# Performance work log

Hardware: AMD Instinct MI355X
Metric: run time of the kernel (lower is better)

Reference implementation:

```python
import jax, jax.numpy as jnp
import numpy as np

# DkNetCL (ConformalLayers): depth x [Conv2d(3x3, pad=1, no bias) + SRePro], then Linear(32768 -> 10).
# ConformalLayers algebraically fuses the cascade in conformal space; the equivalent Euclidean math
# per layer is: x <- conv(x); x <- x * 2*alpha^2 / (2*alpha^2 + ||x||^2), where ||x|| is the l2 norm
# of the ENTIRE flattened feature map of each sample (the sample is a single point in conformal space).
# alpha fixed to 1.0 (cl.SRePro() default is weight-adaptive; a constant keeps the reference deterministic).

DEPTH = 4
ALPHA = 1.0


def _conv(x, w):
    # x: [B, Cin, H, W], w: [Cout, Cin, 3, 3], stride 1, padding 1 (shape-preserving)
    return jax.lax.conv_general_dilated(
        x, w, window_strides=(1, 1), padding=((1, 1), (1, 1)),
        dimension_numbers=("NCHW", "OIHW", "NCHW"))


def _srepro(x, alpha):
    # per-sample squared norm over the whole feature map
    sq = jnp.sum(x * x, axis=(1, 2, 3), keepdims=True)  # [B,1,1,1]
    two_a2 = 2.0 * alpha * alpha
    return x * (two_a2 / (two_a2 + sq))


def setup_inputs() -> dict:
    key = jax.random.key(0)
    ks = jax.random.split(key, DEPTH + 2)
    B, H, W = 1024, 32, 32
    x = jax.random.normal(ks[0], (B, 3, H, W), jnp.float32)
    inp = {"x": x}
    cin = 3
    for i in range(DEPTH):
        fan_in = cin * 9
        inp[f"conv_w{i}"] = jax.random.normal(ks[1 + i], (32, cin, 3, 3), jnp.float32) / np.sqrt(fan_in).astype(np.float32)
        cin = 32
    flat = 32 * H * W  # 32768
    inp["fc_w"] = jax.random.normal(ks[-1], (10, flat), jnp.float32) / np.sqrt(flat).astype(np.float32)
    inp["fc_b"] = jnp.zeros((10,), jnp.float32)
    return inp


def reference(x, conv_w0, conv_w1, conv_w2, conv_w3, fc_w, fc_b):
    for w in (conv_w0, conv_w1, conv_w2, conv_w3):
        x = _srepro(_conv(x, w), ALPHA)
    x = x.reshape(x.shape[0], -1)  # [B, 32768]
    return x @ fc_w.T + fc_b  # [B, 10]
```

## Files before the change

kernel.cpp:

```cpp
#include <hip/hip_runtime.h>
#include <stdint.h>


typedef __bf16 bf16x8 __attribute__((ext_vector_type(8)));
typedef float f32x4 __attribute__((ext_vector_type(4)));
typedef unsigned short u16;
typedef unsigned int u32;

__device__ __forceinline__ u16 f2bf(float f) {
    union { float f; u32 i; } v; v.f = f;
    u32 r = v.i + 0x7FFFu + ((v.i >> 16) & 1u);
    return (u16)(r >> 16);
}
__device__ __forceinline__ float bf2f(u16 u) {
    union { u32 i; float f; } v; v.i = ((u32)u) << 16;
    return v.f;
}
union frag_cast { uint4 u; bf16x8 f; };

__device__ __forceinline__ int swz(int p, int c) {
    return p * 32 + ((c ^ ((p >> 1) & 3)) * 8);
}

__global__ void prep_weights_k(const float* __restrict__ w0, const float* __restrict__ w1,
                               const float* __restrict__ w2, const float* __restrict__ w3,
                               u16* __restrict__ wfrag)
{
    int idx = blockIdx.x * 256 + threadIdx.x;
    if (idx >= 4 * 9 * 2 * 64) return;
    int lane  = idx & 63;
    int mh    = (idx >> 6) & 1;
    int tap   = (idx >> 7) % 9;
    int layer = (idx >> 7) / 9;
    const float* w = layer == 0 ? w0 : layer == 1 ? w1 : layer == 2 ? w2 : w3;
    int cin_act = (layer == 0) ? 3 : 32;
    int cout = mh * 16 + (lane & 15);
    int cin0 = (lane >> 4) * 8;
    int dy = tap / 3, dx = tap % 3;
    u16 v[8];
    for (int j = 0; j < 8; j++) {
        int cin = cin0 + j;
        float f = (cin < cin_act) ? w[((cout * cin_act + cin) * 3 + dy) * 3 + dx] : 0.f;
        v[j] = f2bf(f);
    }
    uint4 pack;
    pack.x = (u32)v[0] | ((u32)v[1] << 16);
    pack.y = (u32)v[2] | ((u32)v[3] << 16);
    pack.z = (u32)v[4] | ((u32)v[5] << 16);
    pack.w = (u32)v[6] | ((u32)v[7] << 16);
    reinterpret_cast<uint4*>(wfrag)[idx] = pack;
}

__global__ void prep_wfc_k(const float* __restrict__ fcw, u16* __restrict__ wfc)
{
    int idx = blockIdx.x * 256 + threadIdx.x;
    int lane = idx & 63, step = idx >> 6;
    int j = lane & 15, kq = lane >> 4;
    u16 hi[8], lo[8];
#pragma unroll
    for (int e = 0; e < 8; e++) {
        int k = step * 32 + kq * 8 + e;
        int c = k & 31, p = k >> 5;
        float f = (j < 10) ? fcw[j * 32768 + c * 1024 + p] : 0.f;
        u16 h = f2bf(f);
        hi[e] = h;
        lo[e] = f2bf(f - bf2f(h));
    }
    uint4 ph, pl;
    ph.x = (u32)hi[0] | ((u32)hi[1] << 16); ph.y = (u32)hi[2] | ((u32)hi[3] << 16);
    ph.z = (u32)hi[4] | ((u32)hi[5] << 16); ph.w = (u32)hi[6] | ((u32)hi[7] << 16);
    pl.x = (u32)lo[0] | ((u32)lo[1] << 16); pl.y = (u32)lo[2] | ((u32)lo[3] << 16);
    pl.z = (u32)lo[4] | ((u32)lo[5] << 16); pl.w = (u32)lo[6] | ((u32)lo[7] << 16);
    reinterpret_cast<uint4*>(wfc)[idx] = ph;
    reinterpret_cast<uint4*>(wfc)[65536 + idx] = pl;
}

__global__ void __launch_bounds__(512, 1)
net_k(const float* __restrict__ x, const u16* __restrict__ wfrag,
      u16* __restrict__ u4, float* __restrict__ c4)
{
    __shared__ u16 lds[2][32768];
    __shared__ float red[8][4];
    const int b = blockIdx.x;
    const int tid = threadIdx.x;
    const int lane = tid & 63;
    const int wv = tid >> 6;
    const int px = lane & 15;
    const int kq = lane >> 4;
    float vn[4] = {0.f, 0.f, 0.f, 0.f};

    const float* xb = x + (size_t)b * 3072;
#pragma unroll
    for (int it = 0; it < 8; it++) {
        int pix = it * 128 + wv * 16 + px;
        int c = kq;
        uint4 val = make_uint4(0, 0, 0, 0);
        if (c == 0) {
            float f0 = xb[pix], f1 = xb[1024 + pix], f2 = xb[2048 + pix];
            val.x = (u32)f2bf(f0) | ((u32)f2bf(f1) << 16);
            val.y = (u32)f2bf(f2);
        }
        *reinterpret_cast<uint4*>(&lds[0][swz(pix, c)]) = val;
    }

    const int orow0 = wv * 4;
#pragma unroll 1
    for (int l = 0; l < 4; l++) {
        bf16x8 W[3][3][2];
        const uint4* wl = reinterpret_cast<const uint4*>(wfrag + l * 9216);
#pragma unroll
        for (int dy = 0; dy < 3; dy++)
#pragma unroll
            for (int dx = 0; dx < 3; dx++)
#pragma unroll
                for (int mh = 0; mh < 2; mh++) {
                    frag_cast fc;
                    fc.u = wl[((dy * 3 + dx) * 2 + mh) * 64 + lane];
                    W[dy][dx][mh] = fc.f;
                }
        const u16* src = lds[l & 1];
        u16* dst = lds[(l & 1) ^ 1];
        __syncthreads();

#pragma unroll 1
        for (int ch = 0; ch < 2; ch++) {
            const int oA = orow0 + ch * 2;
            f32x4 accA[2][2]; f32x4 accB[2][2];
#pragma unroll
            for (int mh = 0; mh < 2; mh++)
#pragma unroll
                for (int nt = 0; nt < 2; nt++) { accA[mh][nt] = (f32x4)0.f; accB[mh][nt] = (f32x4)0.f; }

#pragma unroll
            for (int k = 0; k < 4; k++) {
                int ri = oA - 1 + k;
                if (ri >= 0 && ri < 32) {
                    bf16x8 bfr[2][3];
#pragma unroll
                    for (int nt = 0; nt < 2; nt++)
#pragma unroll
                        for (int d = 0; d < 3; d++) {
                            int xx = nt * 16 + px + d - 1;
                            bool oob = ((unsigned)xx >= 32u);
                            int xc = oob ? (nt * 16 + px) : xx;
                            frag_cast fc;
                            fc.u = *reinterpret_cast<const uint4*>(&src[swz(ri * 32 + xc, kq)]);
                            if (oob) { fc.u.x = 0; fc.u.y = 0; fc.u.z = 0; fc.u.w = 0; }
                            bfr[nt][d] = fc.f;
                        }
                    if (k <= 2) {
#pragma unroll
                        for (int mh = 0; mh < 2; mh++)
#pragma unroll
                            for (int nt = 0; nt < 2; nt++)
#pragma unroll
                                for (int d = 0; d < 3; d++)
                                    accA[mh][nt] = __builtin_amdgcn_mfma_f32_16x16x32_bf16(
                                        W[k][d][mh], bfr[nt][d], accA[mh][nt], 0, 0, 0);
                    }
                    if (k >= 1) {
#pragma unroll
                        for (int mh = 0; mh < 2; mh++)
#pragma unroll
                            for (int nt = 0; nt < 2; nt++)
#pragma unroll
                                for (int d = 0; d < 3; d++)
                                    accB[mh][nt] = __builtin_amdgcn_mfma_f32_16x16x32_bf16(
                                        W[k - 1][d][mh], bfr[nt][d], accB[mh][nt], 0, 0, 0);
                    }
                }
            }
#pragma unroll
            for (int mh = 0; mh < 2; mh++)
#pragma unroll
                for (int nt = 0; nt < 2; nt++) {
                    int cch = mh * 2 + (kq >> 1);
                    int sub = (kq & 1) * 4;
                    f32x4 a = accA[mh][nt];
                    vn[l] += a[0]*a[0] + a[1]*a[1] + a[2]*a[2] + a[3]*a[3];
                    ushort4 h = make_ushort4(f2bf(a[0]), f2bf(a[1]), f2bf(a[2]), f2bf(a[3]));
                    int P0 = oA * 32 + nt * 16 + px;
                    *reinterpret_cast<ushort4*>(&dst[swz(P0, cch) + sub]) = h;
                    f32x4 c = accB[mh][nt];
                    vn[l] += c[0]*c[0] + c[1]*c[1] + c[2]*c[2] + c[3]*c[3];
                    ushort4 h2 = make_ushort4(f2bf(c[0]), f2bf(c[1]), f2bf(c[2]), f2bf(c[3]));
                    int P1 = (oA + 1) * 32 + nt * 16 + px;
                    *reinterpret_cast<ushort4*>(&dst[swz(P1, cch) + sub]) = h2;
                }
        }
    }

#pragma unroll
    for (int l = 0; l < 4; l++)
#pragma unroll
        for (int off = 32; off; off >>= 1) vn[l] += __shfl_xor(vn[l], off);
    if (lane == 0) {
#pragma unroll
        for (int l = 0; l < 4; l++) red[wv][l] = vn[l];
    }
    __syncthreads();
    float c = 1.f;
#pragma unroll
    for (int l = 0; l < 4; l++) {
        float n = 0.f;
#pragma unroll
        for (int w = 0; w < 8; w++) n += red[w][l];
        c = c * (2.f / (2.f + c * c * n));
    }
    if (tid == 0) c4[b] = c;

    u16* ub = u4 + (size_t)b * 32768;
#pragma unroll
    for (int it = 0; it < 8; it++) {
        int pix = it * 128 + wv * 16 + px;
        int cch = kq;
        *reinterpret_cast<uint4*>(ub + pix * 32 + cch * 8) =
            *reinterpret_cast<const uint4*>(&lds[0][swz(pix, cch)]);
    }
}

__global__ void __launch_bounds__(256)
fc_mfma_k(const u16* __restrict__ u4, const u16* __restrict__ wfc,
          float* __restrict__ tmp)
{
    const int lane = threadIdx.x & 63;
    const int wv = threadIdx.x >> 6;
    const int wid = blockIdx.x * 4 + wv;
    const int kc = wid & 31;
    const int st = wid >> 5;
    const int px = lane & 15, kq = lane >> 4;
    const uint4* Ah = reinterpret_cast<const uint4*>(wfc) + kc * 32 * 64 + lane;
    const uint4* Al = Ah + 65536;
    const u16* B = u4 + (size_t)(st * 16 + px) * 32768 + kc * 1024 + kq * 8;
    f32x4 acc = (f32x4)0.f;
#pragma unroll
    for (int s = 0; s < 32; s++) {
        frag_cast a, al, bb;
        a.u  = Ah[s * 64];
        al.u = Al[s * 64];
        bb.u = *reinterpret_cast<const uint4*>(B + s * 32);
        acc = __builtin_amdgcn_mfma_f32_16x16x32_bf16(a.f,  bb.f, acc, 0, 0, 0);
        acc = __builtin_amdgcn_mfma_f32_16x16x32_bf16(al.f, bb.f, acc, 0, 0, 0);
    }
    int sample = st * 16 + px;
#pragma unroll
    for (int r = 0; r < 4; r++) {
        int j = kq * 4 + r;
        if (j < 10) atomicAdd(&tmp[sample * 10 + j], acc[r]);
    }
}

__global__ void finalize_k(const float* __restrict__ tmp, const float* __restrict__ c4,
                           const float* __restrict__ fcb, float* __restrict__ out)
{
    int i = blockIdx.x * 256 + threadIdx.x;
    if (i >= 10240) return;
    int b = i / 10, j = i - b * 10;
    out[i] = c4[b] * tmp[i] + fcb[j];
}

extern "C" void kernel_launch(void* const* d_in, const int* in_sizes, int n_in,
                              void* d_out, int out_size, void* d_ws, size_t ws_size,
                              hipStream_t stream)
{
    const float* x   = (const float*)d_in[0];
    const float* cw0 = (const float*)d_in[1];
    const float* cw1 = (const float*)d_in[2];
    const float* cw2 = (const float*)d_in[3];
    const float* cw3 = (const float*)d_in[4];
    const float* fcw = (const float*)d_in[5];
    const float* fcb = (const float*)d_in[6];
    float* out = (float*)d_out;
    char* ws = (char*)d_ws;

    const size_t USZ = (size_t)1024 * 32768 * 2;
    u16* uA    = (u16*)ws;
    u16* wfrag = (u16*)(ws + USZ);
    u16* wfc   = (u16*)(ws + USZ + 81920);
    float* tmp = (float*)(ws + USZ + 81920 + 2097152);
    float* c4  = tmp + 10240;

    hipMemsetAsync(tmp, 0, 10240 * sizeof(float), stream);
    prep_weights_k<<<18, 256, 0, stream>>>(cw0, cw1, cw2, cw3, wfrag);
    prep_wfc_k<<<256, 256, 0, stream>>>(fcw, wfc);
    net_k<<<1024, 512, 0, stream>>>(x, wfrag, uA, c4);
    fc_mfma_k<<<512, 256, 0, stream>>>(uA, wfc, tmp);
    finalize_k<<<40, 256, 0, stream>>>(tmp, c4, fcb, out);
}
```

Before: 193.3 us.

## Stage FC activation loads through LDS and streamline conv epilogue

The FC kernel now loads activation rows with a coalesced per-row pattern into registers, stages them through a double-buffered swizzled LDS area and prefetches the next chunk while doing MFMAs. It also remaps block indices so blocks sharing a weight slice run together. In the conv kernel, bf16 rounding uses the native cast, the per-layer norm accumulates in a vector register, the channel-chunk loop is unrolled, and out-of-bounds halo reads point at a shared zero slot instead of being masked. These changes target scattered global loads and extra ALU work, at the cost of more LDS use and register pressure. There are no barriers around the LDS buffers, which only works if each wave reads back only the slots that wave itself wrote.

```diff
diff --git a/kernel.cpp b/kernel.cpp
--- a/kernel.cpp
+++ b/kernel.cpp
@@ -15,6 +15,9 @@
 __device__ __forceinline__ float bf2f(u16 u) {
     union { u32 i; float f; } v; v.i = ((u32)u) << 16;
     return v.f;
+}
+__device__ __forceinline__ u16 bfc(float f) {
+    union { __bf16 h; u16 u; } x; x.h = (__bf16)f; return x.u;
 }
 union frag_cast { uint4 u; bf16x8 f; };
 
@@ -81,15 +84,17 @@
 {
     __shared__ u16 lds[2][32768];
     __shared__ float red[8][4];
+    __shared__ uint4 zslot;
     const int b = blockIdx.x;
     const int tid = threadIdx.x;
     const int lane = tid & 63;
     const int wv = tid >> 6;
     const int px = lane & 15;
     const int kq = lane >> 4;
-    float vn[4] = {0.f, 0.f, 0.f, 0.f};
+    float vn[4];
 
     const float* xb = x + (size_t)b * 3072;
+    if (tid == 0) zslot = make_uint4(0, 0, 0, 0);
 #pragma unroll
     for (int it = 0; it < 8; it++) {
         int pix = it * 128 + wv * 16 + px;
@@ -97,8 +102,8 @@
         uint4 val = make_uint4(0, 0, 0, 0);
         if (c == 0) {
             float f0 = xb[pix], f1 = xb[1024 + pix], f2 = xb[2048 + pix];
-            val.x = (u32)f2bf(f0) | ((u32)f2bf(f1) << 16);
-            val.y = (u32)f2bf(f2);
+            val.x = (u32)bfc(f0) | ((u32)bfc(f1) << 16);
+            val.y = (u32)bfc(f2);
         }
         *reinterpret_cast<uint4*>(&lds[0][swz(pix, c)]) = val;
     }
@@ -120,9 +125,10 @@
                 }
         const u16* src = lds[l & 1];
         u16* dst = lds[(l & 1) ^ 1];
+        f32x4 vacc = (f32x4)0.f;
         __syncthreads();
 
-#pragma unroll 1
+#pragma unroll
         for (int ch = 0; ch < 2; ch++) {
             const int oA = orow0 + ch * 2;
             f32x4 accA[2][2]; f32x4 accB[2][2];
@@ -142,10 +148,11 @@
                         for (int d = 0; d < 3; d++) {
                             int xx = nt * 16 + px + d - 1;
                             bool oob = ((unsigned)xx >= 32u);
-                            int xc = oob ? (nt * 16 + px) : xx;
+                            int xs = oob ? (nt * 16 + px) : xx;
+                            const uint4* pr = oob ? &zslot
+                                : reinterpret_cast<const uint4*>(&src[swz(ri * 32 + xs, kq)]);
                             frag_cast fc;
-                            fc.u = *reinterpret_cast<const uint4*>(&src[swz(ri * 32 + xc, kq)]);
-                            if (oob) { fc.u.x = 0; fc.u.y = 0; fc.u.z = 0; fc.u.w = 0; }
+                            fc.u = *pr;
                             bfr[nt][d] = fc.f;
                         }
                     if (k <= 2) {
@@ -177,17 +184,18 @@
                     int cch = mh * 2 + (kq >> 1);
                     int sub = (kq & 1) * 4;
                     f32x4 a = accA[mh][nt];
-                    vn[l] += a[0]*a[0] + a[1]*a[1] + a[2]*a[2] + a[3]*a[3];
-                    ushort4 h = make_ushort4(f2bf(a[0]), f2bf(a[1]), f2bf(a[2]), f2bf(a[3]));
+                    vacc += a * a;
+                    ushort4 h = make_ushort4(bfc(a[0]), bfc(a[1]), bfc(a[2]), bfc(a[3]));
                     int P0 = oA * 32 + nt * 16 + px;
                     *reinterpret_cast<ushort4*>(&dst[swz(P0, cch) + sub]) = h;
                     f32x4 c = accB[mh][nt];
-                    vn[l] += c[0]*c[0] + c[1]*c[1] + c[2]*c[2] + c[3]*c[3];
-                    ushort4 h2 = make_ushort4(f2bf(c[0]), f2bf(c[1]), f2bf(c[2]), f2bf(c[3]));
+                    vacc += c * c;
+                    ushort4 h2 = make_ushort4(bfc(c[0]), bfc(c[1]), bfc(c[2]), bfc(c[3]));
                     int P1 = (oA + 1) * 32 + nt * 16 + px;
                     *reinterpret_cast<ushort4*>(&dst[swz(P1, cch) + sub]) = h2;
                 }
         }
+        vn[l] = vacc[0] + vacc[1] + vacc[2] + vacc[3];
     }
 
 #pragma unroll
@@ -219,28 +227,57 @@
     }
 }
 
+#define FSTG 4
 __global__ void __launch_bounds__(256)
 fc_mfma_k(const u16* __restrict__ u4, const u16* __restrict__ wfc,
           float* __restrict__ tmp)
 {
+    __shared__ uint4 sb[2][4 * FSTG * 64];
     const int lane = threadIdx.x & 63;
     const int wv = threadIdx.x >> 6;
-    const int wid = blockIdx.x * 4 + wv;
+    const int rb = ((blockIdx.x & 7) << 6) + (blockIdx.x >> 3);
+    const int wid = rb * 4 + wv;
     const int kc = wid & 31;
     const int st = wid >> 5;
     const int px = lane & 15, kq = lane >> 4;
+    const int a = lane >> 2, p = lane & 3;
+    const u16* gB = u4 + (size_t)(st * 16 + a) * 32768 + kc * 1024 + p * 8;
+    const int wslot = wv * FSTG * 64 + a * 4 + (p ^ (a & 3));
+    const int rslot = wv * FSTG * 64 + px * 4 + (kq ^ (px & 3));
     const uint4* Ah = reinterpret_cast<const uint4*>(wfc) + kc * 32 * 64 + lane;
     const uint4* Al = Ah + 65536;
-    const u16* B = u4 + (size_t)(st * 16 + px) * 32768 + kc * 1024 + kq * 8;
     f32x4 acc = (f32x4)0.f;
-#pragma unroll
-    for (int s = 0; s < 32; s++) {
-        frag_cast a, al, bb;
-        a.u  = Ah[s * 64];
-        al.u = Al[s * 64];
-        bb.u = *reinterpret_cast<const uint4*>(B + s * 32);
-        acc = __builtin_amdgcn_mfma_f32_16x16x32_bf16(a.f,  bb.f, acc, 0, 0, 0);
-        acc = __builtin_amdgcn_mfma_f32_16x16x32_bf16(al.f, bb.f, acc, 0, 0, 0);
+    uint4 rg[FSTG];
+
+#pragma unroll
+    for (int si = 0; si < FSTG; si++)
+        rg[si] = *reinterpret_cast<const uint4*>(gB + si * 32);
+#pragma unroll
+    for (int si = 0; si < FSTG; si++)
+        sb[0][wslot + si * 64] = rg[si];
+
+#pragma unroll 1
+    for (int c2 = 0; c2 < 8; c2++) {
+        if (c2 < 7) {
+#pragma unroll
+            for (int si = 0; si < FSTG; si++)
+                rg[si] = *reinterpret_cast<const uint4*>(gB + ((c2 + 1) * FSTG + si) * 32);
+        }
+#pragma unroll
+        for (int si = 0; si < FSTG; si++) {
+            int s = c2 * FSTG + si;
+            frag_cast aa, al2, bb;
+            aa.u  = Ah[s * 64];
+            al2.u = Al[s * 64];
+            bb.u  = sb[c2 & 1][rslot + si * 64];
+            acc = __builtin_amdgcn_mfma_f32_16x16x32_bf16(aa.f,  bb.f, acc, 0, 0, 0);
+            acc = __builtin_amdgcn_mfma_f32_16x16x32_bf16(al2.f, bb.f, acc, 0, 0, 0);
+        }
+        if (c2 < 7) {
+#pragma unroll
+            for (int si = 0; si < FSTG; si++)
+                sb[(c2 + 1) & 1][wslot + si * 64] = rg[si];
+        }
     }
     int sample = st * 16 + px;
 #pragma unroll
```

New measurement: 188.0 us. -2.7%, faster.
